# Kernel tuning notes

Measured on AMD Instinct MI355X. Metric: run time of the kernel, lower is better.

The kernel has to match this reference:

```python
import jax, jax.numpy as jnp
import numpy as np

B, C, H, W = 4, 512, 64, 64
CK = C // 8  # key/query channels


def setup_inputs() -> dict:
    key = jax.random.key(0)
    ks = jax.random.split(key, 4)
    x = jax.random.normal(ks[0], (B, C, H, W), dtype=jnp.float32)
    # 1x1 conv weights -> plain [out, in] matrices; fan-in scaled like torch default-ish
    Wf = jax.random.normal(ks[1], (CK, C), dtype=jnp.float32) * (1.0 / np.sqrt(C))
    Wg = jax.random.normal(ks[2], (CK, C), dtype=jnp.float32) * (1.0 / np.sqrt(C))
    Wh = jax.random.normal(ks[3], (C, C), dtype=jnp.float32) * (1.0 / np.sqrt(C))
    bf = jnp.zeros((CK,), dtype=jnp.float32)
    bg = jnp.zeros((CK,), dtype=jnp.float32)
    bh = jnp.zeros((C,), dtype=jnp.float32)
    gamma = jnp.zeros((1,), dtype=jnp.float32)
    return {"x": x, "Wf": Wf, "bf": bf, "Wg": Wg, "bg": bg, "Wh": Wh, "bh": bh, "gamma": gamma}


def reference(x, Wf, bf, Wg, bg, Wh, bh, gamma):
    b, c, h, w = x.shape
    n = h * w
    xf = x.reshape(b, c, n)  # [B, C, N]
    # 1x1 convs == per-pixel linear maps
    f = jnp.einsum('kc,bcn->bkn', Wf, xf) + bf[None, :, None]  # [B, CK, N]
    g = jnp.einsum('kc,bcn->bkn', Wg, xf) + bg[None, :, None]  # [B, CK, N]
    hx = jnp.einsum('oc,bcn->bon', Wh, xf) + bh[None, :, None]  # [B, C, N]
    # energy[b,i,j] = sum_k f[b,k,i] * g[b,k,j]  (f_x.permute(0,2,1) @ g_x)
    energy = jnp.einsum('bki,bkj->bij', f, g)  # [B, N, N]
    attention = jax.nn.softmax(energy, axis=-1)
    # out[b,c,i] = sum_j hx[b,c,j] * attention[b,i,j]  (h_x @ attention^T)
    out = jnp.einsum('bcj,bij->bci', hx, attention)  # [B, C, N]
    out = out.reshape(b, c, h, w)
    return gamma[0] * out + x
```

## Files before the change

### kernel.cpp

```cpp
#include <hip/hip_runtime.h>
#include <hip/hip_bf16.h>

#define NB 4
#define CC 512
#define NN 4096
#define CKK 64

typedef _Float16 f16x4 __attribute__((ext_vector_type(4)));
typedef _Float16 f16x8 __attribute__((ext_vector_type(8)));
typedef float    f32x4 __attribute__((ext_vector_type(4)));

__device__ __forceinline__ void g2l16(const _Float16* g, _Float16* l) {
    __builtin_amdgcn_global_load_lds(
        (const __attribute__((address_space(1))) void*)g,
        (__attribute__((address_space(3))) void*)l, 16, 0, 0);
}

__device__ __forceinline__ void stage_tile(const _Float16* __restrict__ g, int ldg,
                                           _Float16* lds, int lane, int wave) {
    #pragma unroll
    for (int r = 0; r < 2; r++) {
        int q = r * 4 + wave;
        int row = q * 16 + (lane >> 2);
        int col = (lane & 3) * 8;
        g2l16(g + (size_t)row * ldg + col, lds + q * 512 + lane * 8);
    }
}

__launch_bounds__(256)
__global__ void prep(const float* __restrict__ x, _Float16* __restrict__ xT,
                     const float* __restrict__ Wf, const float* __restrict__ bf_,
                     const float* __restrict__ Wg, const float* __restrict__ bg_,
                     const float* __restrict__ Wh, const float* __restrict__ bh_,
                     _Float16* __restrict__ Wall, float* __restrict__ Ball) {
    const int N = NN, C = CC;
    int bid = blockIdx.x;
    int t = threadIdx.x;
    if (bid < 2048) {
        int n0 = (bid & 63) << 6;
        int c0 = ((bid >> 6) & 7) << 6;
        int b  = bid >> 9;
        __shared__ float T[64][65];
        const float* xb = x + (size_t)b * C * N;
        #pragma unroll
        for (int r = 0; r < 4; r++) {
            int c = (t >> 4) + 16 * r;
            int n4 = (t & 15) * 4;
            float4 v = *(const float4*)(xb + (size_t)(c0 + c) * N + n0 + n4);
            T[n4 + 0][c] = v.x; T[n4 + 1][c] = v.y; T[n4 + 2][c] = v.z; T[n4 + 3][c] = v.w;
        }
        __syncthreads();
        int n = t >> 2, cb = (t & 3) * 16;
        f16x8 h0, h1;
        #pragma unroll
        for (int i = 0; i < 8; i++) { h0[i] = (_Float16)T[n][cb + i]; h1[i] = (_Float16)T[n][cb + 8 + i]; }
        _Float16* dst = xT + (size_t)b * N * C + (size_t)(n0 + n) * C + c0 + cb;
        *(f16x8*)dst = h0;
        *(f16x8*)(dst + 8) = h1;
    } else {
        int o = bid - 2048;
        const float* src;
        if (o < 64)       src = Wf + (size_t)o * C;
        else if (o < 128) src = Wg + (size_t)(o - 64) * C;
        else              src = Wh + (size_t)(o - 128) * C;
        Wall[(size_t)o * C + t]       = (_Float16)src[t];
        Wall[(size_t)o * C + 256 + t] = (_Float16)src[256 + t];
        if (t == 0)
            Ball[o] = (o < 64) ? bf_[o] : (o < 128 ? bg_[o - 64] : bh_[o - 128]);
    }
}

__launch_bounds__(256)
__global__ void proj_mfma(const _Float16* __restrict__ xT, const _Float16* __restrict__ Wall,
                          const float* __restrict__ Ball,
                          _Float16* __restrict__ Ft, _Float16* __restrict__ Gt,
                          _Float16* __restrict__ Hx) {
    const int N = NN, C = CC;
    int n0 = blockIdx.x * 128;
    int o0 = blockIdx.y * 128;
    int b  = blockIdx.z;
    const _Float16* Arow = Wall + (size_t)o0 * C;
    const _Float16* Brow = xT + (size_t)b * N * C + (size_t)n0 * C;
    __shared__ _Float16 As[128 * 32];
    __shared__ _Float16 Bs[128 * 32];
    int tid = threadIdx.x, lane = tid & 63, wave = tid >> 6;
    int wm = wave & 1, wn = wave >> 1, lrow = lane & 15, quad = lane >> 4;
    f32x4 acc[4][4] = {};
    for (int kc = 0; kc < C; kc += 32) {
        __syncthreads();
        stage_tile(Arow + kc, C, As, lane, wave);
        stage_tile(Brow + kc, C, Bs, lane, wave);
        __syncthreads();
        f16x8 af[4], bf[4];
        #pragma unroll
        for (int mi = 0; mi < 4; mi++)
            af[mi] = *(const f16x8*)(As + (wm * 64 + mi * 16 + lrow) * 32 + quad * 8);
        #pragma unroll
        for (int ni = 0; ni < 4; ni++)
            bf[ni] = *(const f16x8*)(Bs + (wn * 64 + ni * 16 + lrow) * 32 + quad * 8);
        #pragma unroll
        for (int mi = 0; mi < 4; mi++)
            #pragma unroll
            for (int ni = 0; ni < 4; ni++)
                acc[mi][ni] = __builtin_amdgcn_mfma_f32_16x16x32_f16(af[mi], bf[ni], acc[mi][ni], 0, 0, 0);
    }
    float bias_r[4][4];
    #pragma unroll
    for (int mi = 0; mi < 4; mi++)
        #pragma unroll
        for (int r = 0; r < 4; r++)
            bias_r[mi][r] = Ball[o0 + wm * 64 + mi * 16 + quad * 4 + r];
    _Float16* Ftb = Ft + (size_t)b * NN * CKK;
    _Float16* Gtb = Gt + (size_t)b * NN * CKK;
    _Float16* Hxb = Hx + (size_t)b * CC * N;
    #pragma unroll
    for (int mi = 0; mi < 4; mi++)
        #pragma unroll
        for (int ni = 0; ni < 4; ni++)
            #pragma unroll
            for (int r = 0; r < 4; r++) {
                int o = o0 + wm * 64 + mi * 16 + quad * 4 + r;
                int n = n0 + wn * 64 + ni * 16 + lrow;
                _Float16 v = (_Float16)(acc[mi][ni][r] + bias_r[mi][r]);
                if (o < 64)       Ftb[(size_t)n * CKK + o] = v;
                else if (o < 128) Gtb[(size_t)n * CKK + (o - 64)] = v;
                else              Hxb[(size_t)(o - 128) * N + n] = v;
            }
}

#define PST_LD 136
__launch_bounds__(256)
__global__ void energy_fused(const _Float16* __restrict__ Ft, const _Float16* __restrict__ Gt,
                             _Float16* __restrict__ P, float* __restrict__ Mpart,
                             float* __restrict__ Lpart, int r0, int Rstr) {
    const int N = NN;
    int b = blockIdx.z;
    const _Float16* Arow = Ft + (size_t)b * N * CKK + (size_t)(r0 + blockIdx.y * 128) * CKK;
    const _Float16* Brow = Gt + (size_t)b * N * CKK + (size_t)(blockIdx.x * 128) * CKK;
    _Float16* Pb = P + (size_t)b * Rstr * N + (size_t)blockIdx.y * 128 * N + blockIdx.x * 128;
    __shared__ _Float16 As[128 * 32];
    __shared__ _Float16 Bs[128 * 32];
    __shared__ _Float16 Pst[128 * PST_LD];
    __shared__ float Sred[640];
    int tid = threadIdx.x, lane = tid & 63, wave = tid >> 6;
    int wm = wave & 1, wn = wave >> 1, lrow = lane & 15, quad = lane >> 4;
    f32x4 acc[4][4] = {};
    #pragma unroll
    for (int kc = 0; kc < CKK; kc += 32) {
        __syncthreads();
        stage_tile(Arow + kc, CKK, As, lane, wave);
        stage_tile(Brow + kc, CKK, Bs, lane, wave);
        __syncthreads();
        f16x8 af[4], bf[4];
        #pragma unroll
        for (int mi = 0; mi < 4; mi++)
            af[mi] = *(const f16x8*)(As + (wm * 64 + mi * 16 + lrow) * 32 + quad * 8);
        #pragma unroll
        for (int ni = 0; ni < 4; ni++)
            bf[ni] = *(const f16x8*)(Bs + (wn * 64 + ni * 16 + lrow) * 32 + quad * 8);
        #pragma unroll
        for (int mi = 0; mi < 4; mi++)
            #pragma unroll
            for (int ni = 0; ni < 4; ni++)
                acc[mi][ni] = __builtin_amdgcn_mfma_f32_16x16x32_f16(af[mi], bf[ni], acc[mi][ni], 0, 0, 0);
    }
    float mloc[16];
    #pragma unroll
    for (int mi = 0; mi < 4; mi++)
        #pragma unroll
        for (int r = 0; r < 4; r++) {
            float v = acc[mi][0][r];
            #pragma unroll
            for (int ni = 1; ni < 4; ni++) v = fmaxf(v, acc[mi][ni][r]);
            mloc[mi * 4 + r] = v;
        }
    #pragma unroll
    for (int off = 1; off < 16; off <<= 1)
        #pragma unroll
        for (int s = 0; s < 16; s++)
            mloc[s] = fmaxf(mloc[s], __shfl_xor(mloc[s], off));
    {
        float v = mloc[0];
        #pragma unroll
        for (int s = 1; s < 16; s++) v = (lrow == s) ? mloc[s] : v;
        int row = wm * 64 + (lrow >> 2) * 16 + quad * 4 + (lrow & 3);
        Sred[wn * 128 + row] = v;
    }
    __syncthreads();
    if (tid < 128) Sred[512 + tid] = fmaxf(Sred[tid], Sred[128 + tid]);
    __syncthreads();
    float lloc[16];
    #pragma unroll
    for (int mi = 0; mi < 4; mi++)
        #pragma unroll
        for (int r = 0; r < 4; r++) {
            int row = wm * 64 + mi * 16 + quad * 4 + r;
            float m = Sred[512 + row];
            float s = 0.f;
            #pragma unroll
            for (int ni = 0; ni < 4; ni++) {
                int j = wn * 64 + ni * 16 + lrow;
                float s16 = (float)(_Float16)acc[mi][ni][r];
                _Float16 p16 = (_Float16)__expf(s16 - m);
                Pst[row * PST_LD + j] = p16;
                s += (float)p16;
            }
            lloc[mi * 4 + r] = s;
        }
    #pragma unroll
    for (int off = 1; off < 16; off <<= 1)
        #pragma unroll
        for (int s = 0; s < 16; s++)
            lloc[s] += __shfl_xor(lloc[s], off);
    {
        float v = lloc[0];
        #pragma unroll
        for (int s = 1; s < 16; s++) v = (lrow == s) ? lloc[s] : v;
        int row = wm * 64 + (lrow >> 2) * 16 + quad * 4 + (lrow & 3);
        Sred[256 + wn * 128 + row] = v;
    }
    __syncthreads();
    if (tid < 128) {
        size_t sidx = ((size_t)b * 32 + blockIdx.x) * Rstr + blockIdx.y * 128 + tid;
        Mpart[sidx] = Sred[512 + tid];
        Lpart[sidx] = Sred[256 + tid] + Sred[256 + 128 + tid];
    }
    int col16 = tid & 15, rowb = tid >> 4;
    #pragma unroll
    for (int s = 0; s < 8; s++) {
        int row = rowb + s * 16;
        f16x8 v = *(const f16x8*)(Pst + row * PST_LD + col16 * 8);
        *(f16x8*)(Pb + (size_t)row * N + col16 * 8) = v;
    }
}

__launch_bounds__(256)
__global__ void out_mfma(const _Float16* __restrict__ Hx, const _Float16* __restrict__ P,
                         const float* __restrict__ Mpart, const float* __restrict__ Lpart,
                         const float* __restrict__ x, const float* __restrict__ gamma,
                         float* __restrict__ out, int r0, int Rstr) {
    const int N = NN, C = CC;
    int b = blockIdx.z;
    int i0l = blockIdx.x * 128;
    int c0  = blockIdx.y * 128;
    const _Float16* Arow = Hx + (size_t)b * C * N + (size_t)c0 * N;
    const _Float16* Brow = P  + (size_t)b * Rstr * N + (size_t)i0l * N;
    __shared__ _Float16 As[128 * 32];
    __shared__ _Float16 Bs[128 * 32];
    __shared__ _Float16 Cf[32 * 128];
    int tid = threadIdx.x, lane = tid & 63, wave = tid >> 6;
    int wm = wave & 1, wn = wave >> 1, lrow = lane & 15, quad = lane >> 4;
    if (tid < 128) {
        const float* mp = Mpart + (size_t)b * 32 * Rstr + i0l + tid;
        const float* lp = Lpart + (size_t)b * 32 * Rstr + i0l + tid;
        float mv[32];
        float m = -1e30f;
        #pragma unroll
        for (int jt = 0; jt < 32; jt++) { mv[jt] = mp[(size_t)jt * Rstr]; m = fmaxf(m, mv[jt]); }
        float l = 0.f;
        #pragma unroll
        for (int jt = 0; jt < 32; jt++) {
            float e = __expf(mv[jt] - m);
            mv[jt] = e;
            l += lp[(size_t)jt * Rstr] * e;
        }
        float linv = 1.0f / l;
        #pragma unroll
        for (int jt = 0; jt < 32; jt++)
            Cf[jt * 128 + tid] = (_Float16)(mv[jt] * linv);
    }
    __syncthreads();
    f32x4 acc[4][4] = {};
    for (int jt = 0; jt < 32; jt++) {
        _Float16 cfv[4];
        #pragma unroll
        for (int ni = 0; ni < 4; ni++)
            cfv[ni] = Cf[jt * 128 + wn * 64 + ni * 16 + lrow];
        #pragma unroll
        for (int kk = 0; kk < 4; kk++) {
            int kc = jt * 128 + kk * 32;
            __syncthreads();
            stage_tile(Arow + kc, N, As, lane, wave);
            stage_tile(Brow + kc, N, Bs, lane, wave);
            __syncthreads();
            f16x8 af[4], bf[4];
            #pragma unroll
            for (int mi = 0; mi < 4; mi++)
                af[mi] = *(const f16x8*)(As + (wm * 64 + mi * 16 + lrow) * 32 + quad * 8);
            #pragma unroll
            for (int ni = 0; ni < 4; ni++) {
                bf[ni] = *(const f16x8*)(Bs + (wn * 64 + ni * 16 + lrow) * 32 + quad * 8);
                #pragma unroll
                for (int j = 0; j < 8; j++) bf[ni][j] *= cfv[ni];
            }
            #pragma unroll
            for (int mi = 0; mi < 4; mi++)
                #pragma unroll
                for (int ni = 0; ni < 4; ni++)
                    acc[mi][ni] = __builtin_amdgcn_mfma_f32_16x16x32_f16(af[mi], bf[ni], acc[mi][ni], 0, 0, 0);
        }
    }
    float gv = gamma[0];
    const float* xb = x + (size_t)b * C * N;
    float* ob = out + (size_t)b * C * N;
    int ig0 = r0 + i0l;
    #pragma unroll
    for (int mi = 0; mi < 4; mi++)
        #pragma unroll
        for (int ni = 0; ni < 4; ni++)
            #pragma unroll
            for (int r = 0; r < 4; r++) {
                int c = c0 + wm * 64 + mi * 16 + quad * 4 + r;
                int i = ig0 + wn * 64 + ni * 16 + lrow;
                ob[(size_t)c * N + i] = gv * acc[mi][ni][r] + xb[(size_t)c * N + i];
            }
}

extern "C" void kernel_launch(void* const* d_in, const int* in_sizes, int n_in,
                              void* d_out, int out_size, void* d_ws, size_t ws_size,
                              hipStream_t stream) {
    const float* x     = (const float*)d_in[0];
    const float* Wf    = (const float*)d_in[1];
    const float* bf    = (const float*)d_in[2];
    const float* Wg    = (const float*)d_in[3];
    const float* bg    = (const float*)d_in[4];
    const float* Wh    = (const float*)d_in[5];
    const float* bh    = (const float*)d_in[6];
    const float* gamma = (const float*)d_in[7];
    float* out = (float*)d_out;

    const int B = NB, C = CC, N = NN;

    char* wsb = (char*)d_ws;
    _Float16* Wall = (_Float16*)wsb;
    float*    Ball = (float*)(wsb + ((size_t)768 << 10));
    _Float16* Ft = (_Float16*)(wsb + ((size_t)1 << 20));
    _Float16* Gt = (_Float16*)(wsb + ((size_t)3 << 20));
    _Float16* Hx = (_Float16*)(wsb + ((size_t)5 << 20));
    float* Mpart = (float*)(wsb + ((size_t)21 << 20));
    float* Lpart = (float*)(wsb + ((size_t)23 << 20));
    _Float16* P  = (_Float16*)(wsb + ((size_t)26 << 20));
    _Float16* xT = P;
    size_t base = (size_t)26 << 20;
    size_t avail = (ws_size > base) ? ws_size - base : 0;
    size_t bytesPer128 = (size_t)B * N * 2 * 128;
    int R = (int)(avail / bytesPer128) * 128;
    if (R > N) R = N;
    if (R < 128) R = 128;

    prep<<<dim3(2048 + 640), dim3(256), 0, stream>>>(
        x, xT, Wf, bf, Wg, bg, Wh, bh, Wall, Ball);
    proj_mfma<<<dim3(N / 128, 5, B), dim3(256), 0, stream>>>(xT, Wall, Ball, Ft, Gt, Hx);

    for (int r0 = 0; r0 < N; r0 += R) {
        int rows = (R < N - r0) ? R : (N - r0);
        energy_fused<<<dim3(N / 128, rows / 128, B), dim3(256), 0, stream>>>(
            Ft, Gt, P, Mpart, Lpart, r0, R);
        out_mfma<<<dim3(rows / 128, C / 128, B), dim3(256), 0, stream>>>(
            Hx, P, Mpart, Lpart, x, gamma, out, r0, R);
    }
}
```

Baseline: 268.3 us.

## Fuse energy, softmax and output GEMM into a flash-attention style kernel

Replaces the two-kernel scheme, which wrote the full fp16 probability matrix P to global memory and read it back, with one attn_fused kernel. That kernel computes energy tiles, keeps a running row max and sum (online softmax), rescales the accumulators and multiplies by Hx tiles in LDS. This removes the large P round trip through HBM and the separate Mpart/Lpart partial-statistics reduction. It also adds XOR-swizzled LDS staging and double-buffered Hx loads. In exchange, energy is recomputed once for each of the two 256-channel output slices, the kernel uses about 119KB of dynamic LDS with 512 threads, and each tile adds several barriers.

```diff
diff --git a/kernel.cpp b/kernel.cpp
--- a/kernel.cpp
+++ b/kernel.cpp
@@ -6,7 +6,6 @@
 #define NN 4096
 #define CKK 64
 
-typedef _Float16 f16x4 __attribute__((ext_vector_type(4)));
 typedef _Float16 f16x8 __attribute__((ext_vector_type(8)));
 typedef float    f32x4 __attribute__((ext_vector_type(4)));
 
@@ -25,6 +24,18 @@
         int col = (lane & 3) * 8;
         g2l16(g + (size_t)row * ldg + col, lds + q * 512 + lane * 8);
     }
+}
+
+__device__ __forceinline__ void stage_swz(const _Float16* __restrict__ g, int ldg,
+                                          _Float16* lds, int tid) {
+    int row = tid >> 2;
+    int scq = (tid & 3) ^ ((row >> 1) & 3);
+    g2l16(g + (size_t)row * ldg + scq * 8, lds + tid * 8);
+}
+
+__device__ __forceinline__ f16x8 rd_swz(const _Float16* lds, int row, int quad) {
+    int q = quad ^ ((row >> 1) & 3);
+    return *(const f16x8*)(lds + row * 32 + q * 8);
 }
 
 __launch_bounds__(256)
@@ -128,191 +139,177 @@
             }
 }
 
-#define PST_LD 136
-__launch_bounds__(256)
-__global__ void energy_fused(const _Float16* __restrict__ Ft, const _Float16* __restrict__ Gt,
-                             _Float16* __restrict__ P, float* __restrict__ Mpart,
-                             float* __restrict__ Lpart, int r0, int Rstr) {
-    const int N = NN;
-    int b = blockIdx.z;
-    const _Float16* Arow = Ft + (size_t)b * N * CKK + (size_t)(r0 + blockIdx.y * 128) * CKK;
-    const _Float16* Brow = Gt + (size_t)b * N * CKK + (size_t)(blockIdx.x * 128) * CKK;
-    _Float16* Pb = P + (size_t)b * Rstr * N + (size_t)blockIdx.y * 128 * N + blockIdx.x * 128;
-    __shared__ _Float16 As[128 * 32];
-    __shared__ _Float16 Bs[128 * 32];
-    __shared__ _Float16 Pst[128 * PST_LD];
-    __shared__ float Sred[640];
-    int tid = threadIdx.x, lane = tid & 63, wave = tid >> 6;
-    int wm = wave & 1, wn = wave >> 1, lrow = lane & 15, quad = lane >> 4;
+#define PST_LD  136
+#define MRED_LD 34
+#define SM_FT    0
+#define SM_BSG   16384
+#define SM_PST   32768
+#define SM_AH    67584
+#define SM_MRED  100352
+#define SM_MRUN  117760
+#define SM_LRUN  118272
+#define SM_OSC   118784
+#define SM_TOTAL 119296
+
+__launch_bounds__(512, 2)
+__global__ void attn_fused(const _Float16* __restrict__ Ft, const _Float16* __restrict__ Gt,
+                           const _Float16* __restrict__ Hx, const float* __restrict__ x,
+                           const float* __restrict__ gamma, float* __restrict__ out) {
+    const int N = NN, C = CC;
+    extern __shared__ char smem[];
+    _Float16* FtL = (_Float16*)(smem + SM_FT);
+    _Float16* BsG = (_Float16*)(smem + SM_BSG);
+    _Float16* Pst = (_Float16*)(smem + SM_PST);
+    _Float16* Ah  = (_Float16*)(smem + SM_AH);
+    float* Mred = (float*)(smem + SM_MRED);
+    float* Mrun = (float*)(smem + SM_MRUN);
+    float* Lrun = (float*)(smem + SM_LRUN);
+    float* Osc  = (float*)(smem + SM_OSC);
+
+    const int b  = blockIdx.z;
+    const int i0 = blockIdx.x * 128;
+    const int c0 = blockIdx.y * 256;
+    const int tid = threadIdx.x;
+    const int lane = tid & 63, w = tid >> 6;
+    const int lrow = lane & 15, quad = lane >> 4;
+    const int wi = w & 3, wj = w >> 2;
+    const int wc = w >> 1, wi2 = w & 1;
+
+    const _Float16* Ftb = Ft + (size_t)b * N * CKK + (size_t)i0 * CKK;
+    const _Float16* Gtb = Gt + (size_t)b * N * CKK;
+    const _Float16* Hxb = Hx + (size_t)b * C * N + (size_t)c0 * N;
+
+    stage_swz(Ftb,      CKK, FtL,        tid);
+    stage_swz(Ftb + 32, CKK, FtL + 4096, tid);
+    if (tid < 128) { Mrun[tid] = -1e30f; Lrun[tid] = 0.0f; }
+    __syncthreads();
+
+    f16x8 afs[2][2];
+    #pragma unroll
+    for (int mi = 0; mi < 2; mi++)
+        #pragma unroll
+        for (int ks = 0; ks < 2; ks++)
+            afs[mi][ks] = rd_swz(FtL + ks * 4096, wi * 32 + mi * 16 + lrow, quad);
+
     f32x4 acc[4][4] = {};
-    #pragma unroll
-    for (int kc = 0; kc < CKK; kc += 32) {
-        __syncthreads();
-        stage_tile(Arow + kc, CKK, As, lane, wave);
-        stage_tile(Brow + kc, CKK, Bs, lane, wave);
-        __syncthreads();
-        f16x8 af[4], bf[4];
+
+    for (int jt = 0; jt < NN / 128; jt++) {
+        const _Float16* Gtr = Gtb + (size_t)jt * 128 * CKK;
+        stage_swz(Gtr,      CKK, BsG,        tid);
+        stage_swz(Gtr + 32, CKK, BsG + 4096, tid);
+        __syncthreads();
+
+        f32x4 sacc[2][4] = {};
+        #pragma unroll
+        for (int ks = 0; ks < 2; ks++)
+            #pragma unroll
+            for (int ni = 0; ni < 4; ni++) {
+                f16x8 bfs = rd_swz(BsG + ks * 4096, wj * 64 + ni * 16 + lrow, quad);
+                #pragma unroll
+                for (int mi = 0; mi < 2; mi++)
+                    sacc[mi][ni] = __builtin_amdgcn_mfma_f32_16x16x32_f16(afs[mi][ks], bfs, sacc[mi][ni], 0, 0, 0);
+            }
+        #pragma unroll
+        for (int mi = 0; mi < 2; mi++)
+            #pragma unroll
+            for (int r = 0; r < 4; r++) {
+                float v = fmaxf(fmaxf(sacc[mi][0][r], sacc[mi][1][r]),
+                                fmaxf(sacc[mi][2][r], sacc[mi][3][r]));
+                int row = wi * 32 + mi * 16 + quad * 4 + r;
+                Mred[row * MRED_LD + wj * 16 + lrow] = v;
+            }
+        __syncthreads();
+        if (tid < 128) {
+            const float* mr = Mred + tid * MRED_LD;
+            float mt = mr[0];
+            #pragma unroll
+            for (int k = 1; k < 32; k++) mt = fmaxf(mt, mr[k]);
+            float mo = Mrun[tid];
+            float mn = fmaxf(mo, mt);
+            float sc = __expf(mo - mn);
+            Mrun[tid] = mn;
+            Osc[tid] = sc;
+            Lrun[tid] *= sc;
+        }
+        __syncthreads();
+        #pragma unroll
+        for (int mi = 0; mi < 2; mi++)
+            #pragma unroll
+            for (int r = 0; r < 4; r++) {
+                int row = wi * 32 + mi * 16 + quad * 4 + r;
+                float m = Mrun[row];
+                float ls = 0.f;
+                #pragma unroll
+                for (int ni = 0; ni < 4; ni++) {
+                    float s16 = (float)(_Float16)sacc[mi][ni][r];
+                    _Float16 p16 = (_Float16)__expf(s16 - m);
+                    Pst[row * PST_LD + wj * 64 + ni * 16 + lrow] = p16;
+                    ls += (float)p16;
+                }
+                Mred[row * MRED_LD + wj * 16 + lrow] = ls;
+            }
+        float scv[4];
+        #pragma unroll
+        for (int ni = 0; ni < 4; ni++) scv[ni] = Osc[wi2 * 64 + ni * 16 + lrow];
         #pragma unroll
         for (int mi = 0; mi < 4; mi++)
-            af[mi] = *(const f16x8*)(As + (wm * 64 + mi * 16 + lrow) * 32 + quad * 8);
-        #pragma unroll
-        for (int ni = 0; ni < 4; ni++)
-            bf[ni] = *(const f16x8*)(Bs + (wn * 64 + ni * 16 + lrow) * 32 + quad * 8);
-        #pragma unroll
-        for (int mi = 0; mi < 4; mi++)
             #pragma unroll
             for (int ni = 0; ni < 4; ni++)
-                acc[mi][ni] = __builtin_amdgcn_mfma_f32_16x16x32_f16(af[mi], bf[ni], acc[mi][ni], 0, 0, 0);
-    }
-    float mloc[16];
-    #pragma unroll
-    for (int mi = 0; mi < 4; mi++)
-        #pragma unroll
-        for (int r = 0; r < 4; r++) {
-            float v = acc[mi][0][r];
-            #pragma unroll
-            for (int ni = 1; ni < 4; ni++) v = fmaxf(v, acc[mi][ni][r]);
-            mloc[mi * 4 + r] = v;
+                #pragma unroll
+                for (int r = 0; r < 4; r++)
+                    acc[mi][ni][r] *= scv[ni];
+        __syncthreads();
+        if (tid < 128) {
+            const float* mr = Mred + tid * MRED_LD;
+            float s = 0.f;
+            #pragma unroll
+            for (int k = 0; k < 32; k++) s += mr[k];
+            Lrun[tid] += s;
         }
-    #pragma unroll
-    for (int off = 1; off < 16; off <<= 1)
-        #pragma unroll
-        for (int s = 0; s < 16; s++)
-            mloc[s] = fmaxf(mloc[s], __shfl_xor(mloc[s], off));
-    {
-        float v = mloc[0];
-        #pragma unroll
-        for (int s = 1; s < 16; s++) v = (lrow == s) ? mloc[s] : v;
-        int row = wm * 64 + (lrow >> 2) * 16 + quad * 4 + (lrow & 3);
-        Sred[wn * 128 + row] = v;
+        const _Float16* Hxr = Hxb + (size_t)jt * 128;
+        stage_swz(Hxr,                   N, Ah,        tid);
+        stage_swz(Hxr + (size_t)128 * N, N, Ah + 4096, tid);
+        #pragma unroll
+        for (int kk = 0; kk < 4; kk++) {
+            if (kk < 3) {
+                const _Float16* src = Hxr + (kk + 1) * 32;
+                _Float16* dst = Ah + ((kk + 1) & 1) * 8192;
+                stage_swz(src,                   N, dst,        tid);
+                stage_swz(src + (size_t)128 * N, N, dst + 4096, tid);
+            }
+            __syncthreads();
+            const _Float16* A = Ah + (kk & 1) * 8192;
+            f16x8 bfv[4];
+            #pragma unroll
+            for (int ni = 0; ni < 4; ni++)
+                bfv[ni] = *(const f16x8*)(Pst + (wi2 * 64 + ni * 16 + lrow) * PST_LD + kk * 32 + quad * 8);
+            #pragma unroll
+            for (int mi = 0; mi < 4; mi++) {
+                f16x8 av = rd_swz(A, wc * 64 + mi * 16 + lrow, quad);
+                #pragma unroll
+                for (int ni = 0; ni < 4; ni++)
+                    acc[mi][ni] = __builtin_amdgcn_mfma_f32_16x16x32_f16(av, bfv[ni], acc[mi][ni], 0, 0, 0);
+            }
+        }
     }
     __syncthreads();
-    if (tid < 128) Sred[512 + tid] = fmaxf(Sred[tid], Sred[128 + tid]);
+    if (tid < 128) Osc[tid] = 1.0f / Lrun[tid];
     __syncthreads();
-    float lloc[16];
-    #pragma unroll
-    for (int mi = 0; mi < 4; mi++)
-        #pragma unroll
-        for (int r = 0; r < 4; r++) {
-            int row = wm * 64 + mi * 16 + quad * 4 + r;
-            float m = Sred[512 + row];
-            float s = 0.f;
-            #pragma unroll
-            for (int ni = 0; ni < 4; ni++) {
-                int j = wn * 64 + ni * 16 + lrow;
-                float s16 = (float)(_Float16)acc[mi][ni][r];
-                _Float16 p16 = (_Float16)__expf(s16 - m);
-                Pst[row * PST_LD + j] = p16;
-                s += (float)p16;
-            }
-            lloc[mi * 4 + r] = s;
-        }
-    #pragma unroll
-    for (int off = 1; off < 16; off <<= 1)
-        #pragma unroll
-        for (int s = 0; s < 16; s++)
-            lloc[s] += __shfl_xor(lloc[s], off);
-    {
-        float v = lloc[0];
-        #pragma unroll
-        for (int s = 1; s < 16; s++) v = (lrow == s) ? lloc[s] : v;
-        int row = wm * 64 + (lrow >> 2) * 16 + quad * 4 + (lrow & 3);
-        Sred[256 + wn * 128 + row] = v;
-    }
-    __syncthreads();
-    if (tid < 128) {
-        size_t sidx = ((size_t)b * 32 + blockIdx.x) * Rstr + blockIdx.y * 128 + tid;
-        Mpart[sidx] = Sred[512 + tid];
-        Lpart[sidx] = Sred[256 + tid] + Sred[256 + 128 + tid];
-    }
-    int col16 = tid & 15, rowb = tid >> 4;
-    #pragma unroll
-    for (int s = 0; s < 8; s++) {
-        int row = rowb + s * 16;
-        f16x8 v = *(const f16x8*)(Pst + row * PST_LD + col16 * 8);
-        *(f16x8*)(Pb + (size_t)row * N + col16 * 8) = v;
-    }
-}
-
-__launch_bounds__(256)
-__global__ void out_mfma(const _Float16* __restrict__ Hx, const _Float16* __restrict__ P,
-                         const float* __restrict__ Mpart, const float* __restrict__ Lpart,
-                         const float* __restrict__ x, const float* __restrict__ gamma,
-                         float* __restrict__ out, int r0, int Rstr) {
-    const int N = NN, C = CC;
-    int b = blockIdx.z;
-    int i0l = blockIdx.x * 128;
-    int c0  = blockIdx.y * 128;
-    const _Float16* Arow = Hx + (size_t)b * C * N + (size_t)c0 * N;
-    const _Float16* Brow = P  + (size_t)b * Rstr * N + (size_t)i0l * N;
-    __shared__ _Float16 As[128 * 32];
-    __shared__ _Float16 Bs[128 * 32];
-    __shared__ _Float16 Cf[32 * 128];
-    int tid = threadIdx.x, lane = tid & 63, wave = tid >> 6;
-    int wm = wave & 1, wn = wave >> 1, lrow = lane & 15, quad = lane >> 4;
-    if (tid < 128) {
-        const float* mp = Mpart + (size_t)b * 32 * Rstr + i0l + tid;
-        const float* lp = Lpart + (size_t)b * 32 * Rstr + i0l + tid;
-        float mv[32];
-        float m = -1e30f;
-        #pragma unroll
-        for (int jt = 0; jt < 32; jt++) { mv[jt] = mp[(size_t)jt * Rstr]; m = fmaxf(m, mv[jt]); }
-        float l = 0.f;
-        #pragma unroll
-        for (int jt = 0; jt < 32; jt++) {
-            float e = __expf(mv[jt] - m);
-            mv[jt] = e;
-            l += lp[(size_t)jt * Rstr] * e;
-        }
-        float linv = 1.0f / l;
-        #pragma unroll
-        for (int jt = 0; jt < 32; jt++)
-            Cf[jt * 128 + tid] = (_Float16)(mv[jt] * linv);
-    }
-    __syncthreads();
-    f32x4 acc[4][4] = {};
-    for (int jt = 0; jt < 32; jt++) {
-        _Float16 cfv[4];
-        #pragma unroll
-        for (int ni = 0; ni < 4; ni++)
-            cfv[ni] = Cf[jt * 128 + wn * 64 + ni * 16 + lrow];
-        #pragma unroll
-        for (int kk = 0; kk < 4; kk++) {
-            int kc = jt * 128 + kk * 32;
-            __syncthreads();
-            stage_tile(Arow + kc, N, As, lane, wave);
-            stage_tile(Brow + kc, N, Bs, lane, wave);
-            __syncthreads();
-            f16x8 af[4], bf[4];
-            #pragma unroll
-            for (int mi = 0; mi < 4; mi++)
-                af[mi] = *(const f16x8*)(As + (wm * 64 + mi * 16 + lrow) * 32 + quad * 8);
-            #pragma unroll
-            for (int ni = 0; ni < 4; ni++) {
-                bf[ni] = *(const f16x8*)(Bs + (wn * 64 + ni * 16 + lrow) * 32 + quad * 8);
-                #pragma unroll
-                for (int j = 0; j < 8; j++) bf[ni][j] *= cfv[ni];
-            }
-            #pragma unroll
-            for (int mi = 0; mi < 4; mi++)
-                #pragma unroll
-                for (int ni = 0; ni < 4; ni++)
-                    acc[mi][ni] = __builtin_amdgcn_mfma_f32_16x16x32_f16(af[mi], bf[ni], acc[mi][ni], 0, 0, 0);
-        }
-    }
     float gv = gamma[0];
     const float* xb = x + (size_t)b * C * N;
     float* ob = out + (size_t)b * C * N;
-    int ig0 = r0 + i0l;
+    float li[4];
+    #pragma unroll
+    for (int ni = 0; ni < 4; ni++) li[ni] = Osc[wi2 * 64 + ni * 16 + lrow];
     #pragma unroll
     for (int mi = 0; mi < 4; mi++)
         #pragma unroll
         for (int ni = 0; ni < 4; ni++)
             #pragma unroll
             for (int r = 0; r < 4; r++) {
-                int c = c0 + wm * 64 + mi * 16 + quad * 4 + r;
-                int i = ig0 + wn * 64 + ni * 16 + lrow;
-                ob[(size_t)c * N + i] = gv * acc[mi][ni][r] + xb[(size_t)c * N + i];
+                int c = c0 + wc * 64 + mi * 16 + quad * 4 + r;
+                int i = i0 + wi2 * 64 + ni * 16 + lrow;
+                ob[(size_t)c * N + i] = gv * (acc[mi][ni][r] * li[ni]) + xb[(size_t)c * N + i];
             }
 }
 
@@ -329,34 +326,20 @@
     const float* gamma = (const float*)d_in[7];
     float* out = (float*)d_out;
 
-    const int B = NB, C = CC, N = NN;
-
     char* wsb = (char*)d_ws;
     _Float16* Wall = (_Float16*)wsb;
     float*    Ball = (float*)(wsb + ((size_t)768 << 10));
     _Float16* Ft = (_Float16*)(wsb + ((size_t)1 << 20));
     _Float16* Gt = (_Float16*)(wsb + ((size_t)3 << 20));
     _Float16* Hx = (_Float16*)(wsb + ((size_t)5 << 20));
-    float* Mpart = (float*)(wsb + ((size_t)21 << 20));
-    float* Lpart = (float*)(wsb + ((size_t)23 << 20));
-    _Float16* P  = (_Float16*)(wsb + ((size_t)26 << 20));
-    _Float16* xT = P;
-    size_t base = (size_t)26 << 20;
-    size_t avail = (ws_size > base) ? ws_size - base : 0;
-    size_t bytesPer128 = (size_t)B * N * 2 * 128;
-    int R = (int)(avail / bytesPer128) * 128;
-    if (R > N) R = N;
-    if (R < 128) R = 128;
+    _Float16* xT = (_Float16*)(wsb + ((size_t)21 << 20));
 
     prep<<<dim3(2048 + 640), dim3(256), 0, stream>>>(
         x, xT, Wf, bf, Wg, bg, Wh, bh, Wall, Ball);
-    proj_mfma<<<dim3(N / 128, 5, B), dim3(256), 0, stream>>>(xT, Wall, Ball, Ft, Gt, Hx);
-
-    for (int r0 = 0; r0 < N; r0 += R) {
-        int rows = (R < N - r0) ? R : (N - r0);
-        energy_fused<<<dim3(N / 128, rows / 128, B), dim3(256), 0, stream>>>(
-            Ft, Gt, P, Mpart, Lpart, r0, R);
-        out_mfma<<<dim3(rows / 128, C / 128, B), dim3(256), 0, stream>>>(
-            Hx, P, Mpart, Lpart, x, gamma, out, r0, R);
-    }
-}
+    proj_mfma<<<dim3(NN / 128, 5, NB), dim3(256), 0, stream>>>(xT, Wall, Ball, Ft, Gt, Hx);
+
+    hipFuncSetAttribute((const void*)attn_fused,
+                        hipFuncAttributeMaxDynamicSharedMemorySize, SM_TOTAL);
+    attn_fused<<<dim3(NN / 128, CC / 256, NB), dim3(512), SM_TOTAL, stream>>>(
+        Ft, Gt, Hx, x, gamma, out);
+}
```

New measurement: 275.3 us. 1.03x slower.
